# Kernel tuning notes

Hardware: AMD Instinct MI355X
Metric: run time of the kernel (lower is better)

Reference implementation:

```python
import jax, jax.numpy as jnp
import numpy as np


def setup_inputs() -> dict:
    key = jax.random.key(0)
    ks = jax.random.split(key, 6)
    B, N, d = 8, 2048, 64
    h = jax.random.normal(ks[0], (B, N, d), dtype=jnp.float32)
    adj = jax.random.randint(ks[1], (B, N, N), 0, 2, dtype=jnp.int32)
    h_root = jax.random.normal(ks[2], (B, N), dtype=jnp.float32)
    weight = jax.random.normal(ks[3], (d, d), dtype=jnp.float32) * (1.0 / np.sqrt(d))
    a1 = jax.random.normal(ks[4], (d, 1), dtype=jnp.float32) * (1.0 / np.sqrt(d))
    a2 = jax.random.normal(ks[5], (d, 1), dtype=jnp.float32) * (1.0 / np.sqrt(d))
    return {"h": h, "adj": adj, "h_root": h_root, "weight": weight, "a1": a1, "a2": a2}


def reference(h, adj, h_root, weight, a1, a2):
    h0 = h
    hw = jax.nn.relu(jnp.matmul(h, weight))          # (B,N,d)
    t1 = jnp.matmul(hw, a1)                          # (B,N,1)
    t2 = jnp.matmul(hw, a2)                          # (B,N,1)
    # e[b,i,j] = relu(t1[b,i] + t2[b,j])  (broadcast, same as repeat/view in torch)
    e = jax.nn.relu(t1 + jnp.swapaxes(t2, -1, -2))   # (B,N,N)
    # FAITHFUL to source bug: pos0 = -9e15 * zeros_like(adj) == 0, so
    # non-edges get logit 0 (not -inf) before softmax.
    e = jnp.where(adj > 0, e, jnp.zeros_like(e))
    attention = jax.nn.softmax(e, axis=-1)           # (B,N,N)
    embedding = jnp.matmul(attention, hw)            # (B,N,d)
    # assign = h_root[:,:,None] @ ones(B,1,d) -> h_root broadcast over d;
    # assign > 0  <=>  h_root > 0 since ones are positive.
    assign = h_root[:, :, None] * jnp.ones((1, 1, hw.shape[-1]), dtype=hw.dtype)
    embedding = jnp.where(assign > 0, embedding, h0)
    return embedding
```

## Files before the change

kernel.cpp:

```cpp
#include <hip/hip_runtime.h>
#include <hip/hip_bf16.h>

#define BATCH 8
#define NN    2048
#define DD    64
#define BN    (BATCH * NN)
#define MWORDS 66

typedef __attribute__((ext_vector_type(8))) short bf16x8;
typedef __attribute__((ext_vector_type(4))) float f32x4;

static __device__ __forceinline__ unsigned f2bf_pk(float lo, float hi) {
  unsigned ul = __float_as_uint(lo);
  unsigned uh = __float_as_uint(hi);
  ul = (ul + 0x7fffu + ((ul >> 16) & 1u)) >> 16;
  uh = (uh + 0x7fffu + ((uh >> 16) & 1u)) & 0xffff0000u;
  return ul | uh;
}

__global__ __launch_bounds__(256) void k1_hw_t1_t2(
    const float* __restrict__ h, const float* __restrict__ W,
    const float* __restrict__ a1, const float* __restrict__ a2,
    unsigned short* __restrict__ hwT, float* __restrict__ t1, float* __restrict__ t2) {
  __shared__ float ht[64 * 36];
  __shared__ float Ws[64 * 64];
  __shared__ unsigned short bt[64 * 40];

  const int t  = threadIdx.x;
  const int r0 = blockIdx.x * 32;

#pragma unroll
  for (int r = 0; r < 4; ++r) {
    int f = t + 256 * r;
    reinterpret_cast<float4*>(Ws)[f] = reinterpret_cast<const float4*>(W)[f];
  }
#pragma unroll
  for (int r = 0; r < 2; ++r) {
    int f = t + 256 * r;
    int i = f >> 4, j4 = f & 15;
    float4 v = reinterpret_cast<const float4*>(h + (size_t)(r0 + i) * DD)[j4];
    ht[(4 * j4 + 0) * 36 + i] = v.x;
    ht[(4 * j4 + 1) * 36 + i] = v.y;
    ht[(4 * j4 + 2) * 36 + i] = v.z;
    ht[(4 * j4 + 3) * 36 + i] = v.w;
  }
  __syncthreads();

  const int trow = t >> 4, kcol = t & 15;
  float4 acc0 = make_float4(0.f, 0.f, 0.f, 0.f);
  float4 acc1 = make_float4(0.f, 0.f, 0.f, 0.f);

#pragma unroll 8
  for (int j = 0; j < 64; ++j) {
    float2 hv = *reinterpret_cast<const float2*>(&ht[j * 36 + 2 * trow]);
    float4 wv = reinterpret_cast<const float4*>(Ws)[j * 16 + kcol];
    acc0.x = fmaf(hv.x, wv.x, acc0.x); acc0.y = fmaf(hv.x, wv.y, acc0.y);
    acc0.z = fmaf(hv.x, wv.z, acc0.z); acc0.w = fmaf(hv.x, wv.w, acc0.w);
    acc1.x = fmaf(hv.y, wv.x, acc1.x); acc1.y = fmaf(hv.y, wv.y, acc1.y);
    acc1.z = fmaf(hv.y, wv.z, acc1.z); acc1.w = fmaf(hv.y, wv.w, acc1.w);
  }

  acc0.x = fmaxf(acc0.x, 0.f); acc0.y = fmaxf(acc0.y, 0.f);
  acc0.z = fmaxf(acc0.z, 0.f); acc0.w = fmaxf(acc0.w, 0.f);
  acc1.x = fmaxf(acc1.x, 0.f); acc1.y = fmaxf(acc1.y, 0.f);
  acc1.z = fmaxf(acc1.z, 0.f); acc1.w = fmaxf(acc1.w, 0.f);

  float4 a1v = reinterpret_cast<const float4*>(a1)[kcol];
  float4 a2v = reinterpret_cast<const float4*>(a2)[kcol];
  float s1_0 = acc0.x * a1v.x + acc0.y * a1v.y + acc0.z * a1v.z + acc0.w * a1v.w;
  float s1_1 = acc1.x * a1v.x + acc1.y * a1v.y + acc1.z * a1v.z + acc1.w * a1v.w;
  float s2_0 = acc0.x * a2v.x + acc0.y * a2v.y + acc0.z * a2v.z + acc0.w * a2v.w;
  float s2_1 = acc1.x * a2v.x + acc1.y * a2v.y + acc1.z * a2v.z + acc1.w * a2v.w;
#pragma unroll
  for (int mm = 1; mm <= 8; mm <<= 1) {
    s1_0 += __shfl_xor(s1_0, mm, 64);
    s1_1 += __shfl_xor(s1_1, mm, 64);
    s2_0 += __shfl_xor(s2_0, mm, 64);
    s2_1 += __shfl_xor(s2_1, mm, 64);
  }
  {
    int row = r0 + 2 * trow;
    if (kcol == 0) {
      t1[row] = s1_0; t1[row + 1] = s1_1;
      t2[row] = s2_0; t2[row + 1] = s2_1;
    }
  }

  {
    const float* a0 = &acc0.x;
    const float* a1p = &acc1.x;
#pragma unroll
    for (int c = 0; c < 4; ++c) {
      int k = 4 * kcol + c;
      *reinterpret_cast<unsigned*>(&bt[k * 40 + 2 * trow]) = f2bf_pk(a0[c], a1p[c]);
    }
  }
  __syncthreads();
  {
    int k = t >> 2, jp = t & 3;
    int g = k >> 4, n = k & 15;
    int bb = r0 >> 11;
    int jb = r0 & (NN - 1);
    int ks = jb >> 5;
    size_t base = ((((size_t)bb * (NN / 32) + ks) * 4 + g) * 64 + (jp * 16 + n)) * 8;
    *reinterpret_cast<int4*>(hwT + base) = *reinterpret_cast<const int4*>(&bt[k * 40 + jp * 8]);
  }
}

__global__ __launch_bounds__(256, 4) void k2_attn(
    const unsigned short* __restrict__ hwT, const int* __restrict__ adj,
    const float* __restrict__ t1, const float* __restrict__ t2,
    const float* __restrict__ h, const float* __restrict__ h_root,
    float* __restrict__ out) {
  __shared__ unsigned maskS[16 * MWORDS];
  __shared__ float t2s[NN];
  __shared__ float os[4][16][68];
  __shared__ float denos[4][16];

  const int t    = threadIdx.x;
  const int b    = blockIdx.x >> 7;
  const int i0   = (blockIdx.x & 127) * 16;
  const int w    = t >> 6;
  const int lane = t & 63;
  const int m    = lane & 15;
  const int quad = lane >> 4;

#pragma unroll
  for (int r = 0; r < 2; ++r)
    reinterpret_cast<float4*>(t2s)[t + 256 * r] =
        reinterpret_cast<const float4*>(t2 + b * NN)[t + 256 * r];

  const int rowbase = b * NN + i0;

#pragma unroll 1
  for (int rr = 0; rr < 4; ++rr) {
    const int row = w * 4 + rr;
    const bool active = h_root[rowbase + row] > 0.f;
    if (active) {
      const int* ap = adj + (size_t)(rowbase + row) * NN + lane;
#pragma unroll 1
      for (int sb = 0; sb < 2; ++sb) {
        int v[16];
#pragma unroll
        for (int s = 0; s < 16; ++s) v[s] = ap[(sb * 16 + s) * 64];
#pragma unroll
        for (int s = 0; s < 16; ++s) {
          unsigned long long bal = __ballot(v[s] > 0);
          if (lane == 0)
            *reinterpret_cast<unsigned long long*>(
                &maskS[row * MWORDS + (sb * 16 + s) * 2]) = bal;
        }
      }
    } else {
      maskS[row * MWORDS + lane] = 0u;
    }
  }
  __syncthreads();

  const float t1v = t1[rowbase + m];
  const int ks0 = w * 16;

  f32x4 acc[4];
#pragma unroll
  for (int g = 0; g < 4; ++g) acc[g] = (f32x4){0.f, 0.f, 0.f, 0.f};
  float den = 0.f;

  unsigned mcur = maskS[m * MWORDS + ks0];

#pragma unroll 1
  for (int kk = 0; kk < 16; ++kk) {
    const int ks = ks0 + kk;
    unsigned mnext = 0;
    if (kk + 1 < 16) mnext = maskS[m * MWORDS + ks + 1];

    const unsigned short* bp =
        hwT + ((((size_t)b * (NN / 32) + ks) * 4) * 64 + lane) * 8;
    bf16x8 B0 = *reinterpret_cast<const bf16x8*>(bp);
    bf16x8 B1 = *reinterpret_cast<const bf16x8*>(bp + 512);
    bf16x8 B2 = *reinterpret_cast<const bf16x8*>(bp + 1024);
    bf16x8 B3 = *reinterpret_cast<const bf16x8*>(bp + 1536);

    const float* t2p = &t2s[ks * 32 + quad * 8];
    float4 e0 = *reinterpret_cast<const float4*>(t2p);
    float4 e1 = *reinterpret_cast<const float4*>(t2p + 4);

    const unsigned mm8 = mcur >> (quad * 8);
    float p0 = (mm8 & 1u)   ? __expf(fmaxf(t1v + e0.x, 0.f)) : 1.f;
    float p1 = (mm8 & 2u)   ? __expf(fmaxf(t1v + e0.y, 0.f)) : 1.f;
    float p2 = (mm8 & 4u)   ? __expf(fmaxf(t1v + e0.z, 0.f)) : 1.f;
    float p3 = (mm8 & 8u)   ? __expf(fmaxf(t1v + e0.w, 0.f)) : 1.f;
    float p4 = (mm8 & 16u)  ? __expf(fmaxf(t1v + e1.x, 0.f)) : 1.f;
    float p5 = (mm8 & 32u)  ? __expf(fmaxf(t1v + e1.y, 0.f)) : 1.f;
    float p6 = (mm8 & 64u)  ? __expf(fmaxf(t1v + e1.z, 0.f)) : 1.f;
    float p7 = (mm8 & 128u) ? __expf(fmaxf(t1v + e1.w, 0.f)) : 1.f;
    den += ((p0 + p1) + (p2 + p3)) + ((p4 + p5) + (p6 + p7));

    union { bf16x8 v; unsigned u[4]; } Af;
    Af.u[0] = f2bf_pk(p0, p1); Af.u[1] = f2bf_pk(p2, p3);
    Af.u[2] = f2bf_pk(p4, p5); Af.u[3] = f2bf_pk(p6, p7);

    acc[0] = __builtin_amdgcn_mfma_f32_16x16x32_bf16(Af.v, B0, acc[0], 0, 0, 0);
    acc[1] = __builtin_amdgcn_mfma_f32_16x16x32_bf16(Af.v, B1, acc[1], 0, 0, 0);
    acc[2] = __builtin_amdgcn_mfma_f32_16x16x32_bf16(Af.v, B2, acc[2], 0, 0, 0);
    acc[3] = __builtin_amdgcn_mfma_f32_16x16x32_bf16(Af.v, B3, acc[3], 0, 0, 0);

    mcur = mnext;
  }

  den += __shfl_xor(den, 16, 64);
  den += __shfl_xor(den, 32, 64);
  if (quad == 0) denos[w][m] = den;

#pragma unroll
  for (int g = 0; g < 4; ++g)
#pragma unroll
    for (int r = 0; r < 4; ++r)
      os[w][quad * 4 + r][g * 16 + m] = acc[g][r];
  __syncthreads();

  {
    const int i = t >> 4, k4 = t & 15;
    float4 a = make_float4(0.f, 0.f, 0.f, 0.f);
    float d = 0.f;
#pragma unroll
    for (int ww = 0; ww < 4; ++ww) {
      float4 p = *reinterpret_cast<const float4*>(&os[ww][i][k4 * 4]);
      a.x += p.x; a.y += p.y; a.z += p.z; a.w += p.w;
      d += denos[ww][i];
    }
    const size_t row = (size_t)rowbase + i;
    float4 res;
    if (h_root[row] > 0.f) {
      const float inv = 1.f / d;
      res.x = a.x * inv; res.y = a.y * inv; res.z = a.z * inv; res.w = a.w * inv;
    } else {
      res = reinterpret_cast<const float4*>(h + row * DD)[k4];
    }
    reinterpret_cast<float4*>(out + row * DD)[k4] = res;
  }
}

extern "C" void kernel_launch(void* const* d_in, const int* in_sizes, int n_in,
                              void* d_out, int out_size, void* d_ws, size_t ws_size,
                              hipStream_t stream) {
  const float* h      = (const float*)d_in[0];
  const int*   adj    = (const int*)d_in[1];
  const float* h_root = (const float*)d_in[2];
  const float* W      = (const float*)d_in[3];
  const float* a1     = (const float*)d_in[4];
  const float* a2     = (const float*)d_in[5];
  float* out = (float*)d_out;

  unsigned short* hwT = (unsigned short*)d_ws;
  float* t1 = (float*)(hwT + (size_t)BN * DD);
  float* t2 = t1 + BN;

  k1_hw_t1_t2<<<BN / 32, 256, 0, stream>>>(h, W, a1, a2, hwT, t1, t2);
  k2_attn<<<BATCH * (NN / 16), 256, 0, stream>>>(hwT, adj, t1, t2, h, h_root, out);
}
```

Before: 210.2 us.

## Compact active rows into per-batch list so attention blocks skip inactive work

The first kernel now builds a per-batch list of rows with positive h_root using atomics and copies h into the output for inactive rows. The attention kernel processes only the compacted active rows, so roughly half the blocks exit immediately instead of doing the full MFMA loop over all columns with zero masks. This adds a memset launch and atomics, and makes the row order within a block nondeterministic.

```diff
diff --git a/kernel.cpp b/kernel.cpp
--- a/kernel.cpp
+++ b/kernel.cpp
@@ -21,13 +21,16 @@
 __global__ __launch_bounds__(256) void k1_hw_t1_t2(
     const float* __restrict__ h, const float* __restrict__ W,
     const float* __restrict__ a1, const float* __restrict__ a2,
-    unsigned short* __restrict__ hwT, float* __restrict__ t1, float* __restrict__ t2) {
+    const float* __restrict__ h_root,
+    unsigned short* __restrict__ hwT, float* __restrict__ t1, float* __restrict__ t2,
+    int* __restrict__ counts, int* __restrict__ list, float* __restrict__ out) {
   __shared__ float ht[64 * 36];
   __shared__ float Ws[64 * 64];
   __shared__ unsigned short bt[64 * 40];
 
   const int t  = threadIdx.x;
   const int r0 = blockIdx.x * 32;
+  const int bb = r0 >> 11;
 
 #pragma unroll
   for (int r = 0; r < 4; ++r) {
@@ -95,11 +98,28 @@
       *reinterpret_cast<unsigned*>(&bt[k * 40 + 2 * trow]) = f2bf_pk(a0[c], a1p[c]);
     }
   }
+
+  if (t < 32) {
+    int row = r0 + t;
+    if (h_root[row] > 0.f) {
+      int idx = atomicAdd(&counts[bb], 1);
+      list[bb * NN + idx] = row;
+    }
+  }
+#pragma unroll
+  for (int r = 0; r < 2; ++r) {
+    int f = t + 256 * r;
+    int i = f >> 4, k4 = f & 15;
+    int row = r0 + i;
+    if (h_root[row] <= 0.f)
+      reinterpret_cast<float4*>(out + (size_t)row * DD)[k4] =
+          reinterpret_cast<const float4*>(h + (size_t)row * DD)[k4];
+  }
+
   __syncthreads();
   {
     int k = t >> 2, jp = t & 3;
     int g = k >> 4, n = k & 15;
-    int bb = r0 >> 11;
     int jb = r0 & (NN - 1);
     int ks = jb >> 5;
     size_t base = ((((size_t)bb * (NN / 32) + ks) * 4 + g) * 64 + (jp * 16 + n)) * 8;
@@ -110,34 +130,41 @@
 __global__ __launch_bounds__(256, 4) void k2_attn(
     const unsigned short* __restrict__ hwT, const int* __restrict__ adj,
     const float* __restrict__ t1, const float* __restrict__ t2,
-    const float* __restrict__ h, const float* __restrict__ h_root,
+    const int* __restrict__ counts, const int* __restrict__ list,
     float* __restrict__ out) {
   __shared__ unsigned maskS[16 * MWORDS];
   __shared__ float t2s[NN];
   __shared__ float os[4][16][68];
   __shared__ float denos[4][16];
+  __shared__ int rowsS[16];
 
   const int t    = threadIdx.x;
   const int b    = blockIdx.x >> 7;
-  const int i0   = (blockIdx.x & 127) * 16;
+  const int sblk = blockIdx.x & 127;
+  const int nact = counts[b];
+  if (sblk * 16 >= nact) return;
+
   const int w    = t >> 6;
   const int lane = t & 63;
   const int m    = lane & 15;
   const int quad = lane >> 4;
 
+  if (t < 16) {
+    int s = sblk * 16 + t;
+    rowsS[t] = (s < nact) ? list[b * NN + s] : -1;
+  }
 #pragma unroll
   for (int r = 0; r < 2; ++r)
     reinterpret_cast<float4*>(t2s)[t + 256 * r] =
         reinterpret_cast<const float4*>(t2 + b * NN)[t + 256 * r];
-
-  const int rowbase = b * NN + i0;
+  __syncthreads();
 
 #pragma unroll 1
   for (int rr = 0; rr < 4; ++rr) {
-    const int row = w * 4 + rr;
-    const bool active = h_root[rowbase + row] > 0.f;
-    if (active) {
-      const int* ap = adj + (size_t)(rowbase + row) * NN + lane;
+    const int slot = w * 4 + rr;
+    const int row  = rowsS[slot];
+    if (row >= 0) {
+      const int* ap = adj + (size_t)row * NN + lane;
 #pragma unroll 1
       for (int sb = 0; sb < 2; ++sb) {
         int v[16];
@@ -148,16 +175,17 @@
           unsigned long long bal = __ballot(v[s] > 0);
           if (lane == 0)
             *reinterpret_cast<unsigned long long*>(
-                &maskS[row * MWORDS + (sb * 16 + s) * 2]) = bal;
+                &maskS[slot * MWORDS + (sb * 16 + s) * 2]) = bal;
         }
       }
     } else {
-      maskS[row * MWORDS + lane] = 0u;
-    }
-  }
-  __syncthreads();
-
-  const float t1v = t1[rowbase + m];
+      maskS[slot * MWORDS + lane] = 0u;
+    }
+  }
+  __syncthreads();
+
+  const int arow = rowsS[m];
+  const float t1v = (arow >= 0) ? t1[arow] : 0.f;
   const int ks0 = w * 16;
 
   f32x4 acc[4];
@@ -220,23 +248,21 @@
 
   {
     const int i = t >> 4, k4 = t & 15;
-    float4 a = make_float4(0.f, 0.f, 0.f, 0.f);
-    float d = 0.f;
-#pragma unroll
-    for (int ww = 0; ww < 4; ++ww) {
-      float4 p = *reinterpret_cast<const float4*>(&os[ww][i][k4 * 4]);
-      a.x += p.x; a.y += p.y; a.z += p.z; a.w += p.w;
-      d += denos[ww][i];
-    }
-    const size_t row = (size_t)rowbase + i;
-    float4 res;
-    if (h_root[row] > 0.f) {
+    const int row = rowsS[i];
+    if (row >= 0) {
+      float4 a = make_float4(0.f, 0.f, 0.f, 0.f);
+      float d = 0.f;
+#pragma unroll
+      for (int ww = 0; ww < 4; ++ww) {
+        float4 p = *reinterpret_cast<const float4*>(&os[ww][i][k4 * 4]);
+        a.x += p.x; a.y += p.y; a.z += p.z; a.w += p.w;
+        d += denos[ww][i];
+      }
       const float inv = 1.f / d;
+      float4 res;
       res.x = a.x * inv; res.y = a.y * inv; res.z = a.z * inv; res.w = a.w * inv;
-    } else {
-      res = reinterpret_cast<const float4*>(h + row * DD)[k4];
-    }
-    reinterpret_cast<float4*>(out + row * DD)[k4] = res;
+      reinterpret_cast<float4*>(out + (size_t)row * DD)[k4] = res;
+    }
   }
 }
 
@@ -254,7 +280,11 @@
   unsigned short* hwT = (unsigned short*)d_ws;
   float* t1 = (float*)(hwT + (size_t)BN * DD);
   float* t2 = t1 + BN;
-
-  k1_hw_t1_t2<<<BN / 32, 256, 0, stream>>>(h, W, a1, a2, hwT, t1, t2);
-  k2_attn<<<BATCH * (NN / 16), 256, 0, stream>>>(hwT, adj, t1, t2, h, h_root, out);
-}
+  int* counts = (int*)(t2 + BN);
+  int* list = counts + BATCH;
+
+  hipMemsetAsync(counts, 0, BATCH * sizeof(int), stream);
+  k1_hw_t1_t2<<<BN / 32, 256, 0, stream>>>(h, W, a1, a2, h_root, hwT, t1, t2,
+                                           counts, list, out);
+  k2_attn<<<BATCH * 128, 256, 0, stream>>>(hwT, adj, t1, t2, counts, list, out);
+}
```

Result: slower. 216.6 us (+3.1%).

## Split adjacency bitmask packing into a separate pre-pass kernel

Applied to the files above, without the earlier changes.

Adds a kpack kernel that reads each active adjacency row with 128-bit loads and packs it into 64 32-bit mask words in workspace. The attention kernel then loads its 16 rows of packed masks with one int4 per thread, replacing the strided scalar loads and ballots it did before. The aim is to pull the memory-bound read of the large int32 adjacency tensor out of the compute-heavy, occupancy-limited attention kernel so it can run at full bandwidth. The cost is an extra launch and a small mask round trip through global memory. Inactive rows keep uninitialised mask words, but their outputs are replaced by h0 anyway.

```diff
diff --git a/kernel.cpp b/kernel.cpp
--- a/kernel.cpp
+++ b/kernel.cpp
@@ -5,7 +5,7 @@
 #define NN    2048
 #define DD    64
 #define BN    (BATCH * NN)
-#define MWORDS 66
+#define MWORDS 68
 
 typedef __attribute__((ext_vector_type(8))) short bf16x8;
 typedef __attribute__((ext_vector_type(4))) float f32x4;
@@ -16,6 +16,25 @@
   ul = (ul + 0x7fffu + ((ul >> 16) & 1u)) >> 16;
   uh = (uh + 0x7fffu + ((uh >> 16) & 1u)) & 0xffff0000u;
   return ul | uh;
+}
+
+__global__ __launch_bounds__(256) void kpack(
+    const int* __restrict__ adj, const float* __restrict__ h_root,
+    unsigned* __restrict__ masks) {
+  const int row  = blockIdx.x * 4 + (threadIdx.x >> 6);
+  const int lane = threadIdx.x & 63;
+  if (h_root[row] <= 0.f) return;
+  const int* ap = adj + (size_t)row * NN + lane * 32;
+  unsigned word = 0;
+#pragma unroll
+  for (int i = 0; i < 8; ++i) {
+    int4 v = *reinterpret_cast<const int4*>(ap + i * 4);
+    word |= (v.x > 0 ? 1u : 0u) << (i * 4 + 0);
+    word |= (v.y > 0 ? 1u : 0u) << (i * 4 + 1);
+    word |= (v.z > 0 ? 1u : 0u) << (i * 4 + 2);
+    word |= (v.w > 0 ? 1u : 0u) << (i * 4 + 3);
+  }
+  masks[(size_t)row * 64 + lane] = word;
 }
 
 __global__ __launch_bounds__(256) void k1_hw_t1_t2(
@@ -108,7 +127,7 @@
 }
 
 __global__ __launch_bounds__(256, 4) void k2_attn(
-    const unsigned short* __restrict__ hwT, const int* __restrict__ adj,
+    const unsigned short* __restrict__ hwT, const unsigned* __restrict__ masks,
     const float* __restrict__ t1, const float* __restrict__ t2,
     const float* __restrict__ h, const float* __restrict__ h_root,
     float* __restrict__ out) {
@@ -124,36 +143,18 @@
   const int lane = t & 63;
   const int m    = lane & 15;
   const int quad = lane >> 4;
+  const int rowbase = b * NN + i0;
 
 #pragma unroll
   for (int r = 0; r < 2; ++r)
     reinterpret_cast<float4*>(t2s)[t + 256 * r] =
         reinterpret_cast<const float4*>(t2 + b * NN)[t + 256 * r];
 
-  const int rowbase = b * NN + i0;
-
-#pragma unroll 1
-  for (int rr = 0; rr < 4; ++rr) {
-    const int row = w * 4 + rr;
-    const bool active = h_root[rowbase + row] > 0.f;
-    if (active) {
-      const int* ap = adj + (size_t)(rowbase + row) * NN + lane;
-#pragma unroll 1
-      for (int sb = 0; sb < 2; ++sb) {
-        int v[16];
-#pragma unroll
-        for (int s = 0; s < 16; ++s) v[s] = ap[(sb * 16 + s) * 64];
-#pragma unroll
-        for (int s = 0; s < 16; ++s) {
-          unsigned long long bal = __ballot(v[s] > 0);
-          if (lane == 0)
-            *reinterpret_cast<unsigned long long*>(
-                &maskS[row * MWORDS + (sb * 16 + s) * 2]) = bal;
-        }
-      }
-    } else {
-      maskS[row * MWORDS + lane] = 0u;
-    }
+  {
+    int row = t >> 4, w4 = t & 15;
+    int4 mv = *reinterpret_cast<const int4*>(
+        masks + ((size_t)(rowbase + row)) * 64 + w4 * 4);
+    *reinterpret_cast<int4*>(&maskS[row * MWORDS + w4 * 4]) = mv;
   }
   __syncthreads();
 
@@ -254,7 +255,9 @@
   unsigned short* hwT = (unsigned short*)d_ws;
   float* t1 = (float*)(hwT + (size_t)BN * DD);
   float* t2 = t1 + BN;
-
+  unsigned* masks = (unsigned*)(t2 + BN);
+
+  kpack<<<BN / 4, 256, 0, stream>>>(adj, h_root, masks);
   k1_hw_t1_t2<<<BN / 32, 256, 0, stream>>>(h, W, a1, a2, hwT, t1, t2);
-  k2_attn<<<BATCH * (NN / 16), 256, 0, stream>>>(hwT, adj, t1, t2, h, h_root, out);
-}
+  k2_attn<<<BATCH * (NN / 16), 256, 0, stream>>>(hwT, masks, t1, t2, h, h_root, out);
+}
```

New measurement: 214.9 us. +2.2%, slower.

## Process 32 rows per attention block with 512 threads and interleave batches

Applied to the files above, without the earlier changes.

The attention kernel now handles 32 query rows per block using 8 waves: two 16-row groups, each split across four key-range waves. The intent is to reuse the staged t2 vector and the bf16 hw tiles across more rows per block, halving the number of blocks. The block-to-batch mapping is interleaved so consecutive blocks hit different batches, and the mask row stride changes to 68. Larger blocks with four-per-CU launch bounds put more pressure on registers and LDS, and may reduce occupancy.

```diff
diff --git a/kernel.cpp b/kernel.cpp
--- a/kernel.cpp
+++ b/kernel.cpp
@@ -5,7 +5,7 @@
 #define NN    2048
 #define DD    64
 #define BN    (BATCH * NN)
-#define MWORDS 66
+#define MWORDS 68
 
 typedef __attribute__((ext_vector_type(8))) short bf16x8;
 typedef __attribute__((ext_vector_type(4))) float f32x4;
@@ -63,7 +63,7 @@
   acc0.x = fmaxf(acc0.x, 0.f); acc0.y = fmaxf(acc0.y, 0.f);
   acc0.z = fmaxf(acc0.z, 0.f); acc0.w = fmaxf(acc0.w, 0.f);
   acc1.x = fmaxf(acc1.x, 0.f); acc1.y = fmaxf(acc1.y, 0.f);
-  acc1.z = fmaxf(acc1.z, 0.f); acc1.w = fmaxf(acc1.w, 0.f);
+  acc1.w = fmaxf(acc1.w, 0.f); acc1.z = fmaxf(acc1.z, 0.f);
 
   float4 a1v = reinterpret_cast<const float4*>(a1)[kcol];
   float4 a2v = reinterpret_cast<const float4*>(a2)[kcol];
@@ -107,30 +107,26 @@
   }
 }
 
-__global__ __launch_bounds__(256, 4) void k2_attn(
+__global__ __launch_bounds__(512, 4) void k2_attn(
     const unsigned short* __restrict__ hwT, const int* __restrict__ adj,
     const float* __restrict__ t1, const float* __restrict__ t2,
     const float* __restrict__ h, const float* __restrict__ h_root,
     float* __restrict__ out) {
-  __shared__ unsigned maskS[16 * MWORDS];
+  __shared__ unsigned maskS[32 * MWORDS];
   __shared__ float t2s[NN];
-  __shared__ float os[4][16][68];
-  __shared__ float denos[4][16];
+  __shared__ float os[8][16][68];
+  __shared__ float denos[8][16];
 
   const int t    = threadIdx.x;
-  const int b    = blockIdx.x >> 7;
-  const int i0   = (blockIdx.x & 127) * 16;
+  const int b    = blockIdx.x & 7;
+  const int i0   = (blockIdx.x >> 3) * 32;
   const int w    = t >> 6;
   const int lane = t & 63;
   const int m    = lane & 15;
   const int quad = lane >> 4;
-
-#pragma unroll
-  for (int r = 0; r < 2; ++r)
-    reinterpret_cast<float4*>(t2s)[t + 256 * r] =
-        reinterpret_cast<const float4*>(t2 + b * NN)[t + 256 * r];
-
   const int rowbase = b * NN + i0;
+
+  reinterpret_cast<float4*>(t2s)[t] = reinterpret_cast<const float4*>(t2 + b * NN)[t];
 
 #pragma unroll 1
   for (int rr = 0; rr < 4; ++rr) {
@@ -157,21 +153,24 @@
   }
   __syncthreads();
 
-  const float t1v = t1[rowbase + m];
-  const int ks0 = w * 16;
+  const int g2 = w >> 2;
+  const int jq = w & 3;
+  const int ks0 = jq * 16;
+  const int mrow = g2 * 16 + m;
+  const float t1v = t1[rowbase + mrow];
 
   f32x4 acc[4];
 #pragma unroll
   for (int g = 0; g < 4; ++g) acc[g] = (f32x4){0.f, 0.f, 0.f, 0.f};
   float den = 0.f;
 
-  unsigned mcur = maskS[m * MWORDS + ks0];
+  unsigned mcur = maskS[mrow * MWORDS + ks0];
 
 #pragma unroll 1
   for (int kk = 0; kk < 16; ++kk) {
     const int ks = ks0 + kk;
     unsigned mnext = 0;
-    if (kk + 1 < 16) mnext = maskS[m * MWORDS + ks + 1];
+    if (kk + 1 < 16) mnext = maskS[mrow * MWORDS + ks + 1];
 
     const unsigned short* bp =
         hwT + ((((size_t)b * (NN / 32) + ks) * 4) * 64 + lane) * 8;
@@ -219,24 +218,26 @@
   __syncthreads();
 
   {
-    const int i = t >> 4, k4 = t & 15;
+    const int row = t >> 4, k4 = t & 15;
+    const int wb = (row >> 4) * 4;
+    const int rl = row & 15;
     float4 a = make_float4(0.f, 0.f, 0.f, 0.f);
     float d = 0.f;
 #pragma unroll
     for (int ww = 0; ww < 4; ++ww) {
-      float4 p = *reinterpret_cast<const float4*>(&os[ww][i][k4 * 4]);
+      float4 p = *reinterpret_cast<const float4*>(&os[wb + ww][rl][k4 * 4]);
       a.x += p.x; a.y += p.y; a.z += p.z; a.w += p.w;
-      d += denos[ww][i];
-    }
-    const size_t row = (size_t)rowbase + i;
+      d += denos[wb + ww][rl];
+    }
+    const size_t rowA = (size_t)rowbase + row;
     float4 res;
-    if (h_root[row] > 0.f) {
+    if (h_root[rowA] > 0.f) {
       const float inv = 1.f / d;
       res.x = a.x * inv; res.y = a.y * inv; res.z = a.z * inv; res.w = a.w * inv;
     } else {
-      res = reinterpret_cast<const float4*>(h + row * DD)[k4];
-    }
-    reinterpret_cast<float4*>(out + row * DD)[k4] = res;
+      res = reinterpret_cast<const float4*>(h + rowA * DD)[k4];
+    }
+    reinterpret_cast<float4*>(out + rowA * DD)[k4] = res;
   }
 }
 
@@ -256,5 +257,5 @@
   float* t2 = t1 + BN;
 
   k1_hw_t1_t2<<<BN / 32, 256, 0, stream>>>(h, W, a1, a2, hwT, t1, t2);
-  k2_attn<<<BATCH * (NN / 16), 256, 0, stream>>>(hwT, adj, t1, t2, h, h_root, out);
-}
+  k2_attn<<<BN / 32, 512, 0, stream>>>(hwT, adj, t1, t2, h, h_root, out);
+}
```

Result: no change. 210.9 us (+0.3%).
